# Optimization experiments

Hardware: AMD Instinct MI355X
Metric: run time of the kernel (lower is better)

## Reference

```python
import jax, jax.numpy as jnp
import numpy as np

B, L, N = 8, 512, 512          # batch, seq_len, d_model (= n_nodes)
ND = 10                        # node_dim
CC, SC = 16, 16                # conv_channel, skip_channel
GDEP = 2
ALPHA = 0.05
TOPK = 4
LN_EPS = 1e-5


def setup_inputs() -> dict:
    key = jax.random.key(0)
    ks = jax.random.split(key, 9)
    return {
        "x": jax.random.normal(ks[0], (B, L, N), jnp.float32),
        "nodevec": jax.random.normal(ks[1], (N, ND), jnp.float32),
        "nodeveck": jax.random.normal(ks[2], (1, ND), jnp.float32),
        "w_start": jax.random.normal(ks[3], (CC, 1), jnp.float32) * 0.1,
        "b_start": jax.random.normal(ks[4], (CC,), jnp.float32) * 0.1,
        "w_mlp": jax.random.normal(ks[5], (SC, (GDEP + 1) * CC), jnp.float32) * 0.1,
        "b_mlp": jax.random.normal(ks[6], (SC,), jnp.float32) * 0.1,
        "w_end": jax.random.normal(ks[7], (1, SC), jnp.float32) * 0.1,
        "b_end": jax.random.normal(ks[8], (1,), jnp.float32) * 0.1,
        "ln_gamma": jnp.ones((N,), jnp.float32),
        "ln_beta": jnp.zeros((N,), jnp.float32),
    }


def _conv1x1(h, w, b):
    # h: [B, Cin, N, L], w: [Cout, Cin], b: [Cout]
    return jnp.einsum('bcnl,oc->bonl', h, w) + b[None, :, None, None]


def reference(x, nodevec, nodeveck, w_start, b_start, w_mlp, b_mlp,
              w_end, b_end, ln_gamma, ln_beta):
    n = x.shape[-1]
    # --- learned adjacency + top-k masking ---
    nv = nodevec * nodeveck                         # [N, node_dim]
    adj0 = jax.nn.softmax(jax.nn.relu(nv @ nv.T), axis=1)  # [N, N]
    _, idx = jax.lax.top_k(adj0, TOPK)              # [N, k]
    rows = jnp.arange(n)[:, None]
    mask = jnp.zeros((n, n), x.dtype).at[rows, idx].set(1.0)
    adj = adj0 * mask
    # --- mixprop row normalization (with self loops) ---
    adj = adj + jnp.eye(n, dtype=x.dtype)
    a = adj / adj.sum(axis=1, keepdims=True)        # [N, N]
    # --- start 1x1 conv: x [B,L,N] -> [B,1,N,L] -> [B,CC,N,L] ---
    h0 = jnp.transpose(x[:, None], (0, 1, 3, 2))
    h0 = _conv1x1(h0, w_start, b_start)
    # --- gdep-depth diffusion: h_v <- alpha*h0 + (1-alpha) * sum_w a[v,w] h_w ---
    h = h0
    outs = [h0]
    for _ in range(GDEP):
        h = ALPHA * h0 + (1.0 - ALPHA) * jnp.einsum('bcwl,vw->bcvl', h, a)
        outs.append(h)
    ho = jnp.concatenate(outs, axis=1)              # [B,(gdep+1)*CC,N,L]
    ho = _conv1x1(ho, w_mlp, b_mlp)                 # [B,SC,N,L]
    ho = jax.nn.gelu(ho, approximate=False)
    out = _conv1x1(ho, w_end, b_end)                # [B,1,N,L]
    out = jnp.transpose(out[:, 0], (0, 2, 1))       # [B,L,N]
    # --- residual + LayerNorm over last dim ---
    y = x + out
    mu = jnp.mean(y, axis=-1, keepdims=True)
    var = jnp.var(y, axis=-1, keepdims=True)
    return (y - mu) / jnp.sqrt(var + LN_EPS) * ln_gamma + ln_beta
```

## Files before the change

kernel.cpp:

```cpp
#include <hip/hip_runtime.h>
#include <math.h>

#define N_NODES 512
#define BATCH   8
#define SEQ     512
#define NDIM    10
#define CC      16
#define SC      16
#define TOPK    4
#define ALPHA   0.05f
#define LN_EPS  1e-5f
#define ROWS_PER_BLOCK 4

#define OFF_NW    2048
#define OFF_WSELF 4096
#define OFF_U     4608
#define OFF_BETA  4656
#define OFF_WEND  4672
#define OFF_BEND  4688
#define N_CONST   81

__device__ __forceinline__ float gelu_exact_fast(float t) {
    const float z = fabsf(t) * 0.70710678118654752440f;
    const float e = __expf(-0.5f * t * t);
    const float r = __builtin_amdgcn_rcpf(fmaf(0.3275911f, z, 1.0f));
    float p = fmaf(1.061405429f, r, -1.453152027f);
    p = fmaf(p, r, 1.421413741f);
    p = fmaf(p, r, -0.284496736f);
    p = fmaf(p, r, 0.254829592f);
    p = p * r;
    const float erfz = 1.0f - p * e;
    return 0.5f * t * (1.0f + copysignf(erfz, t));
}

__global__ __launch_bounds__(64) void prep_kernel(
    const float* __restrict__ nodevec,
    const float* __restrict__ nodeveck,
    const float* __restrict__ w_start,
    const float* __restrict__ b_start,
    const float* __restrict__ w_mlp,
    const float* __restrict__ b_mlp,
    const float* __restrict__ w_end,
    const float* __restrict__ b_end,
    int*   __restrict__ wsI,
    float* __restrict__ wsF)
{
    const int v    = blockIdx.x;
    const int lane = threadIdx.x;

    if (v == N_NODES) {
        if (lane < SC) {
            const int o = lane;
            float u0 = 0.f, u1 = 0.f, u2 = 0.f, bt = b_mlp[o];
            for (int c = 0; c < CC; ++c) {
                const float ws = w_start[c];
                const float bs = b_start[c];
                const float m0 = w_mlp[o * 48 + c];
                const float m1 = w_mlp[o * 48 + 16 + c];
                const float m2 = w_mlp[o * 48 + 32 + c];
                u0 += m0 * ws; u1 += m1 * ws; u2 += m2 * ws;
                bt += (m0 + m1 + m2) * bs;
            }
            wsF[OFF_U + 0 * 16 + o] = u0;
            wsF[OFF_U + 1 * 16 + o] = u1;
            wsF[OFF_U + 2 * 16 + o] = u2;
            wsF[OFF_BETA + o]       = bt;
            wsF[OFF_WEND + o]       = w_end[o];
            if (o == 0) wsF[OFF_BEND] = b_end[0];
        }
        return;
    }

    float q[NDIM];
    #pragma unroll
    for (int d = 0; d < NDIM; ++d) {
        const float k = nodeveck[d];
        q[d] = nodevec[v * NDIM + d] * k * k;
    }

    float s[8];
    int   wi[8];
    #pragma unroll
    for (int j = 0; j < 8; ++j) {
        const int w = lane + 64 * j;
        wi[j] = w;
        float dot = 0.f;
        #pragma unroll
        for (int d = 0; d < NDIM; ++d) dot += q[d] * nodevec[w * NDIM + d];
        s[j] = dot > 0.f ? dot : 0.f;
    }

    float m = s[0];
    #pragma unroll
    for (int j = 1; j < 8; ++j) m = fmaxf(m, s[j]);
    for (int off = 32; off; off >>= 1) m = fmaxf(m, __shfl_down(m, off));
    m = __shfl(m, 0);

    float zs = 0.f;
    #pragma unroll
    for (int j = 0; j < 8; ++j) zs += expf(s[j] - m);
    for (int off = 32; off; off >>= 1) zs += __shfl_down(zs, off);
    zs = __shfl(zs, 0);

    float sl[8];
    #pragma unroll
    for (int j = 0; j < 8; ++j) sl[j] = s[j];

    float topv[TOPK];
    int   topi[TOPK];
    for (int t = 0; t < TOPK; ++t) {
        float bv = -1.f; int bi = N_NODES;
        #pragma unroll
        for (int j = 0; j < 8; ++j) {
            if (sl[j] > bv || (sl[j] == bv && wi[j] < bi)) { bv = sl[j]; bi = wi[j]; }
        }
        for (int off = 32; off; off >>= 1) {
            const float ov = __shfl_down(bv, off);
            const int   oi = __shfl_down(bi, off);
            if (ov > bv || (ov == bv && oi < bi)) { bv = ov; bi = oi; }
        }
        bv = __shfl(bv, 0); bi = __shfl(bi, 0);
        topv[t] = bv; topi[t] = bi;
        #pragma unroll
        for (int j = 0; j < 8; ++j) if (wi[j] == bi) sl[j] = -1.f;
    }

    if (lane == 0) {
        float p[TOPK], rs = 1.f;
        #pragma unroll
        for (int t = 0; t < TOPK; ++t) { p[t] = expf(topv[t] - m) / zs; rs += p[t]; }
        const float inv = 1.f / rs;
        #pragma unroll
        for (int t = 0; t < TOPK; ++t) {
            wsI[t * N_NODES + v]          = topi[t];
            wsF[OFF_NW + t * N_NODES + v] = p[t] * inv;
        }
        wsF[OFF_WSELF + v] = inv;
    }
}

__global__ __launch_bounds__(512) void graphblock_kernel(
    const float* __restrict__ x,
    const float* __restrict__ ln_gamma,
    const float* __restrict__ ln_beta,
    const int*   __restrict__ wsI,
    const float* __restrict__ wsF,
    float*       __restrict__ out)
{
    __shared__ float s_x0[N_NODES];
    __shared__ float s_x1[N_NODES];
    __shared__ float s_c[N_CONST];
    __shared__ float s_red[16];

    const int tid  = threadIdx.x;
    const int row0 = blockIdx.x * ROWS_PER_BLOCK;

    if (tid < N_CONST) s_c[tid] = wsF[OFF_U + tid];

    const int   i0 = wsI[0 * N_NODES + tid];
    const int   i1 = wsI[1 * N_NODES + tid];
    const int   i2 = wsI[2 * N_NODES + tid];
    const int   i3 = wsI[3 * N_NODES + tid];
    const float a0 = wsF[OFF_NW + 0 * N_NODES + tid];
    const float a1 = wsF[OFF_NW + 1 * N_NODES + tid];
    const float a2 = wsF[OFF_NW + 2 * N_NODES + tid];
    const float a3 = wsF[OFF_NW + 3 * N_NODES + tid];
    const float as = wsF[OFF_WSELF + tid];
    const float gam = ln_gamma[tid];
    const float bet = ln_beta[tid];

    const float one_m_alpha = 1.f - ALPHA;

    for (int r = 0; r < ROWS_PER_BLOCK; ++r) {
        const size_t row = (size_t)(row0 + r);
        const float x0 = x[row * N_NODES + tid];
        s_x0[tid] = x0;
        __syncthreads();

        float g = a0 * s_x0[i0] + a1 * s_x0[i1] + a2 * s_x0[i2] + a3 * s_x0[i3] + as * x0;
        const float x1 = ALPHA * x0 + one_m_alpha * g;
        s_x1[tid] = x1;
        __syncthreads();

        g = a0 * s_x1[i0] + a1 * s_x1[i1] + a2 * s_x1[i2] + a3 * s_x1[i3] + as * x1;
        const float x2 = ALPHA * x0 + one_m_alpha * g;

        float acc = s_c[80];
        #pragma unroll
        for (int o = 0; o < SC; ++o) {
            const float t = s_c[o] * x0 + s_c[16 + o] * x1 + s_c[32 + o] * x2 + s_c[48 + o];
            acc += s_c[64 + o] * gelu_exact_fast(t);
        }

        const float y = x0 + acc;

        float sum = y, sumsq = y * y;
        for (int off = 32; off; off >>= 1) {
            sum   += __shfl_down(sum, off);
            sumsq += __shfl_down(sumsq, off);
        }
        const int wv = tid >> 6;
        if ((tid & 63) == 0) { s_red[wv] = sum; s_red[8 + wv] = sumsq; }
        __syncthreads();

        float ts = 0.f, tq = 0.f;
        #pragma unroll
        for (int i = 0; i < 8; ++i) { ts += s_red[i]; tq += s_red[8 + i]; }
        const float mu   = ts * (1.f / (float)N_NODES);
        const float var  = tq * (1.f / (float)N_NODES) - mu * mu;
        const float rstd = 1.0f / sqrtf(var + LN_EPS);

        out[row * N_NODES + tid] = (y - mu) * rstd * gam + bet;
    }
}

extern "C" void kernel_launch(void* const* d_in, const int* in_sizes, int n_in,
                              void* d_out, int out_size, void* d_ws, size_t ws_size,
                              hipStream_t stream) {
    const float* x        = (const float*)d_in[0];
    const float* nodevec  = (const float*)d_in[1];
    const float* nodeveck = (const float*)d_in[2];
    const float* w_start  = (const float*)d_in[3];
    const float* b_start  = (const float*)d_in[4];
    const float* w_mlp    = (const float*)d_in[5];
    const float* b_mlp    = (const float*)d_in[6];
    const float* w_end    = (const float*)d_in[7];
    const float* b_end    = (const float*)d_in[8];
    const float* ln_gamma = (const float*)d_in[9];
    const float* ln_beta  = (const float*)d_in[10];

    int*   wsI = (int*)d_ws;
    float* wsF = (float*)d_ws;

    prep_kernel<<<N_NODES + 1, 64, 0, stream>>>(
        nodevec, nodeveck, w_start, b_start, w_mlp, b_mlp, w_end, b_end, wsI, wsF);

    graphblock_kernel<<<(BATCH * SEQ) / ROWS_PER_BLOCK, 512, 0, stream>>>(
        x, ln_gamma, ln_beta, (const int*)d_ws, (const float*)d_ws, (float*)d_out);
}
```

Measured before the change: 108.0 us.

## Map one row per wavefront to drop block-level barriers in graph block kernel

Restructures the main kernel so each 64-lane wavefront processes a whole 512-node row, with eight nodes per lane, instead of a 512-thread block processing four rows. The diffusion steps now go through a per-wave LDS buffer using wave barriers, and LayerNorm uses only a wave shuffle reduction, so the block-wide __syncthreads calls go away. Neighbor indices are packed into 16-bit pairs, and MLP constants are read from global memory rather than staged in LDS. The trade-off is higher register pressure and fewer rows in flight per block, and the small grid of 1024 blocks of 256 threads may limit occupancy.

Measured after the change: 107.5 us. Within noise of the previous version (-0.4%).

```diff
diff --git a/kernel.cpp b/kernel.cpp
--- a/kernel.cpp
+++ b/kernel.cpp
@@ -10,7 +10,8 @@
 #define TOPK    4
 #define ALPHA   0.05f
 #define LN_EPS  1e-5f
-#define ROWS_PER_BLOCK 4
+#define WAVES_PER_BLOCK 4
+#define NODES_PER_LANE  8
 
 #define OFF_NW    2048
 #define OFF_WSELF 4096
@@ -18,7 +19,6 @@
 #define OFF_BETA  4656
 #define OFF_WEND  4672
 #define OFF_BEND  4688
-#define N_CONST   81
 
 __device__ __forceinline__ float gelu_exact_fast(float t) {
     const float z = fabsf(t) * 0.70710678118654752440f;
@@ -139,7 +139,7 @@
     }
 }
 
-__global__ __launch_bounds__(512) void graphblock_kernel(
+__global__ __launch_bounds__(256, 4) void graphblock_kernel(
     const float* __restrict__ x,
     const float* __restrict__ ln_gamma,
     const float* __restrict__ ln_beta,
@@ -147,70 +147,100 @@
     const float* __restrict__ wsF,
     float*       __restrict__ out)
 {
-    __shared__ float s_x0[N_NODES];
-    __shared__ float s_x1[N_NODES];
-    __shared__ float s_c[N_CONST];
-    __shared__ float s_red[16];
+    __shared__ float lds[WAVES_PER_BLOCK * 2 * N_NODES];
 
     const int tid  = threadIdx.x;
-    const int row0 = blockIdx.x * ROWS_PER_BLOCK;
-
-    if (tid < N_CONST) s_c[tid] = wsF[OFF_U + tid];
-
-    const int   i0 = wsI[0 * N_NODES + tid];
-    const int   i1 = wsI[1 * N_NODES + tid];
-    const int   i2 = wsI[2 * N_NODES + tid];
-    const int   i3 = wsI[3 * N_NODES + tid];
-    const float a0 = wsF[OFF_NW + 0 * N_NODES + tid];
-    const float a1 = wsF[OFF_NW + 1 * N_NODES + tid];
-    const float a2 = wsF[OFF_NW + 2 * N_NODES + tid];
-    const float a3 = wsF[OFF_NW + 3 * N_NODES + tid];
-    const float as = wsF[OFF_WSELF + tid];
-    const float gam = ln_gamma[tid];
-    const float bet = ln_beta[tid];
-
-    const float one_m_alpha = 1.f - ALPHA;
-
-    for (int r = 0; r < ROWS_PER_BLOCK; ++r) {
-        const size_t row = (size_t)(row0 + r);
-        const float x0 = x[row * N_NODES + tid];
-        s_x0[tid] = x0;
-        __syncthreads();
-
-        float g = a0 * s_x0[i0] + a1 * s_x0[i1] + a2 * s_x0[i2] + a3 * s_x0[i3] + as * x0;
-        const float x1 = ALPHA * x0 + one_m_alpha * g;
-        s_x1[tid] = x1;
-        __syncthreads();
-
-        g = a0 * s_x1[i0] + a1 * s_x1[i1] + a2 * s_x1[i2] + a3 * s_x1[i3] + as * x1;
-        const float x2 = ALPHA * x0 + one_m_alpha * g;
-
-        float acc = s_c[80];
+    const int lane = tid & 63;
+    const int wid  = tid >> 6;
+    const int row  = blockIdx.x * WAVES_PER_BLOCK + wid;
+
+    float* buf0 = &lds[wid * 2 * N_NODES];
+    float* buf1 = buf0 + N_NODES;
+
+    const float* xr = x + (size_t)row * N_NODES;
+
+    float x0[NODES_PER_LANE];
+    unsigned int p01[NODES_PER_LANE], p23[NODES_PER_LANE];
+    float a0[NODES_PER_LANE], a1[NODES_PER_LANE], a2[NODES_PER_LANE],
+          a3[NODES_PER_LANE], asf[NODES_PER_LANE];
+
+    #pragma unroll
+    for (int j = 0; j < NODES_PER_LANE; ++j) {
+        const int v = j * 64 + lane;
+        x0[j] = xr[v];
+        const unsigned int i0 = (unsigned int)wsI[0 * N_NODES + v];
+        const unsigned int i1 = (unsigned int)wsI[1 * N_NODES + v];
+        const unsigned int i2 = (unsigned int)wsI[2 * N_NODES + v];
+        const unsigned int i3 = (unsigned int)wsI[3 * N_NODES + v];
+        p01[j] = i0 | (i1 << 16);
+        p23[j] = i2 | (i3 << 16);
+        a0[j]  = wsF[OFF_NW + 0 * N_NODES + v];
+        a1[j]  = wsF[OFF_NW + 1 * N_NODES + v];
+        a2[j]  = wsF[OFF_NW + 2 * N_NODES + v];
+        a3[j]  = wsF[OFF_NW + 3 * N_NODES + v];
+        asf[j] = wsF[OFF_WSELF + v];
+        buf0[v] = x0[j];
+    }
+    asm volatile("s_waitcnt lgkmcnt(0)" ::: "memory");
+    __builtin_amdgcn_wave_barrier();
+
+    const float OMA = 1.f - ALPHA;
+
+    float x1[NODES_PER_LANE];
+    #pragma unroll
+    for (int j = 0; j < NODES_PER_LANE; ++j) {
+        const float g = a0[j] * buf0[p01[j] & 0xffffu]
+                      + a1[j] * buf0[p01[j] >> 16]
+                      + a2[j] * buf0[p23[j] & 0xffffu]
+                      + a3[j] * buf0[p23[j] >> 16]
+                      + asf[j] * x0[j];
+        x1[j] = ALPHA * x0[j] + OMA * g;
+        buf1[j * 64 + lane] = x1[j];
+    }
+    asm volatile("s_waitcnt lgkmcnt(0)" ::: "memory");
+    __builtin_amdgcn_wave_barrier();
+
+    const float bend = wsF[OFF_BEND];
+
+    float yv[NODES_PER_LANE];
+    #pragma unroll
+    for (int j = 0; j < NODES_PER_LANE; ++j) {
+        const float g = a0[j] * buf1[p01[j] & 0xffffu]
+                      + a1[j] * buf1[p01[j] >> 16]
+                      + a2[j] * buf1[p23[j] & 0xffffu]
+                      + a3[j] * buf1[p23[j] >> 16]
+                      + asf[j] * x1[j];
+        const float x2 = ALPHA * x0[j] + OMA * g;
+
+        float acc = bend;
         #pragma unroll
         for (int o = 0; o < SC; ++o) {
-            const float t = s_c[o] * x0 + s_c[16 + o] * x1 + s_c[32 + o] * x2 + s_c[48 + o];
-            acc += s_c[64 + o] * gelu_exact_fast(t);
-        }
-
-        const float y = x0 + acc;
-
-        float sum = y, sumsq = y * y;
-        for (int off = 32; off; off >>= 1) {
-            sum   += __shfl_down(sum, off);
-            sumsq += __shfl_down(sumsq, off);
-        }
-        const int wv = tid >> 6;
-        if ((tid & 63) == 0) { s_red[wv] = sum; s_red[8 + wv] = sumsq; }
-        __syncthreads();
-
-        float ts = 0.f, tq = 0.f;
-        #pragma unroll
-        for (int i = 0; i < 8; ++i) { ts += s_red[i]; tq += s_red[8 + i]; }
-        const float mu   = ts * (1.f / (float)N_NODES);
-        const float var  = tq * (1.f / (float)N_NODES) - mu * mu;
-        const float rstd = 1.0f / sqrtf(var + LN_EPS);
-
-        out[row * N_NODES + tid] = (y - mu) * rstd * gam + bet;
+            const float t = wsF[OFF_U + o]          * x0[j]
+                          + wsF[OFF_U + 16 + o]     * x1[j]
+                          + wsF[OFF_U + 32 + o]     * x2
+                          + wsF[OFF_BETA + o];
+            acc = fmaf(wsF[OFF_WEND + o], gelu_exact_fast(t), acc);
+        }
+        yv[j] = x0[j] + acc;
+    }
+
+    float s = 0.f, q = 0.f;
+    #pragma unroll
+    for (int j = 0; j < NODES_PER_LANE; ++j) { s += yv[j]; q += yv[j] * yv[j]; }
+    #pragma unroll
+    for (int off = 32; off; off >>= 1) {
+        s += __shfl_xor(s, off);
+        q += __shfl_xor(q, off);
+    }
+    const float mu   = s * (1.f / (float)N_NODES);
+    const float var  = q * (1.f / (float)N_NODES) - mu * mu;
+    const float rstd = 1.0f / sqrtf(var + LN_EPS);
+
+    float* orow = out + (size_t)row * N_NODES;
+    #pragma unroll
+    for (int j = 0; j < NODES_PER_LANE; ++j) {
+        const int v = j * 64 + lane;
+        orow[v] = (yv[j] - mu) * rstd * ln_gamma[v] + ln_beta[v];
     }
 }
 
@@ -235,6 +265,6 @@
     prep_kernel<<<N_NODES + 1, 64, 0, stream>>>(
         nodevec, nodeveck, w_start, b_start, w_mlp, b_mlp, w_end, b_end, wsI, wsF);
 
-    graphblock_kernel<<<(BATCH * SEQ) / ROWS_PER_BLOCK, 512, 0, stream>>>(
+    graphblock_kernel<<<(BATCH * SEQ) / WAVES_PER_BLOCK, 256, 0, stream>>>(
         x, ln_gamma, ln_beta, (const int*)d_ws, (const float*)d_ws, (float*)d_out);
 }
```
